# Performance work log

Hardware: AMD Instinct MI355X
Metric: run time of the kernel (lower is better)

The kernel has to match this reference:

```python
import jax, jax.numpy as jnp
import numpy as np

N = 100_000      # nodes
E = 1_600_000    # edges (before self-loops)
F_IN = 128       # num_features
H = 128          # nhid
G = 512          # graphs in batch
C = 10           # num_classes
EPS = 1e-5       # BatchNorm eps


def setup_inputs() -> dict:
    key = jax.random.key(0)
    ks = jax.random.split(key, 24)
    x = jax.random.normal(ks[0], (N, F_IN), jnp.float32)
    edge_index = jax.random.randint(ks[1], (2, E), 0, N, dtype=jnp.int64)
    batch = jnp.sort(jax.random.randint(ks[2], (N,), 0, G, dtype=jnp.int64))

    def lin(k, fi, fo):
        return jax.random.normal(k, (fi, fo), jnp.float32) / np.sqrt(fi).astype(np.float32)

    inp = dict(x=x, edge_index=edge_index, batch=batch)
    inp.update(
        W1=lin(ks[3], F_IN, H), b1=jnp.zeros((H,), jnp.float32),
        g1=jnp.ones((H,), jnp.float32), be1=jnp.zeros((H,), jnp.float32),
        W2=lin(ks[4], H, H), b2=jnp.zeros((H,), jnp.float32),
        g2=jnp.ones((H,), jnp.float32), be2=jnp.zeros((H,), jnp.float32),
        W3=lin(ks[5], H, H), b3=jnp.zeros((H,), jnp.float32),
        g3=jnp.ones((H,), jnp.float32), be3=jnp.zeros((H,), jnp.float32),
        gp=jnp.ones((H,), jnp.float32), bep=jnp.zeros((H,), jnp.float32),
        lw1=lin(ks[6], H, H), lb1=jnp.zeros((H,), jnp.float32),
        lw2=lin(ks[7], H, C), lb2=jnp.zeros((C,), jnp.float32),
    )
    return inp


def _batchnorm(h, g, b):
    # training-mode BatchNorm1d: batch stats, biased variance
    m = h.mean(axis=0)
    v = h.var(axis=0)
    return g * (h - m) * jax.lax.rsqrt(v + EPS) + b


def _gcn(h, W, b, src, dst, norm, n):
    # GCNConv: h @ W, then normalized gather-scatter aggregation
    h = h @ W
    msg = h[src] * norm[:, None]                     # [E+N, H] gather
    out = jax.ops.segment_sum(msg, dst, num_segments=n)
    return out + b


def reference(x, edge_index, batch, W1, b1, g1, be1, W2, b2, g2, be2,
              W3, b3, g3, be3, gp, bep, lw1, lb1, lw2, lb2):
    n = x.shape[0]
    loops = jnp.arange(n, dtype=edge_index.dtype)
    src = jnp.concatenate([edge_index[0], loops])
    dst = jnp.concatenate([edge_index[1], loops])
    # symmetric normalization D^{-1/2} (A+I) D^{-1/2}
    deg = jax.ops.segment_sum(jnp.ones_like(src, dtype=x.dtype), dst, num_segments=n)
    dis = jnp.where(deg > 0, jax.lax.rsqrt(jnp.maximum(deg, 1.0)), 0.0)
    norm = dis[src] * dis[dst]

    h = jax.nn.relu(_batchnorm(_gcn(x, W1, b1, src, dst, norm, n), g1, be1))
    h = jax.nn.relu(_batchnorm(_gcn(h, W2, b2, src, dst, norm, n), g2, be2))
    h = jax.nn.relu(_batchnorm(_gcn(h, W3, b3, src, dst, norm, n), g3, be3))

    # global_mean_pool over graph ids
    counts = jax.ops.segment_sum(jnp.ones((n,), x.dtype), batch, num_segments=G)
    pooled = jax.ops.segment_sum(h, batch, num_segments=G) / jnp.maximum(counts, 1.0)[:, None]

    z = _batchnorm(pooled, gp, bep)
    z = jax.nn.relu(z @ lw1 + lb1)
    # dropout_ratio=0.0 -> identity
    z = z @ lw2 + lb2
    return jax.nn.log_softmax(z, axis=-1)
```

## Files before the change

### kernel.cpp

```cpp
#include <hip/hip_runtime.h>
#include <hip/hip_bf16.h>
#include <cstdint>

#define HDIM 128

typedef __bf16 bf16x8 __attribute__((ext_vector_type(8)));
typedef unsigned short usx8 __attribute__((ext_vector_type(8)));
typedef float fx4 __attribute__((ext_vector_type(4)));

__device__ __forceinline__ float bf2f(unsigned short u) {
    unsigned int x = ((unsigned int)u) << 16;
    return __uint_as_float(x);
}
__device__ __forceinline__ unsigned short f2bf(float f) {
    unsigned int x = __float_as_uint(f);
    x += 0x7fffu + ((x >> 16) & 1u);
    return (unsigned short)(x >> 16);
}

__device__ __forceinline__ void detect_local(const unsigned int* xw, const unsigned int* eiw,
                                             int& f0, int& f1) {
    int sane = 0;
    for (int k = 0; k < 64; k++) {
        unsigned int w = xw[k];
        unsigned short ss[2] = {(unsigned short)(w & 0xffffu), (unsigned short)(w >> 16)};
        for (int q = 0; q < 2; q++) {
            int e = (ss[q] >> 7) & 0xFF;
            if ((ss[q] & 0x7fffu) == 0 || (e >= 100 && e <= 140)) sane++;
        }
    }
    f0 = (sane >= 110) ? 1 : 0;
    int zeros = 0;
    for (int k = 1; k < 64; k += 2)
        if (eiw[k] == 0) zeros++;
    f1 = (zeros >= 24) ? 1 : 0;
}

struct ParamTab {
    const void* p[15];
    int n[15];
    int off[15];
};

__global__ void phase1(const unsigned int* __restrict__ xw, const unsigned int* __restrict__ eiw,
                       const void* __restrict__ ei, const void* __restrict__ batch,
                       const void* __restrict__ W1, const void* __restrict__ W2,
                       const void* __restrict__ W3, ParamTab tab, int* __restrict__ flags,
                       float* __restrict__ gsumAll, int* __restrict__ Ct,
                       unsigned short* __restrict__ wconv, unsigned short* __restrict__ Wf,
                       int* __restrict__ goff, int* __restrict__ gcnt, int E, int N, int G,
                       int NB, int ntiles, int TILE) {
    __shared__ int h[1024];
    __shared__ int lf0s, lf1s;
    int b = blockIdx.x, t = threadIdx.x;
    if (t == 0) {
        int a0, a1;
        detect_local(xw, eiw, a0, a1);
        lf0s = a0;
        lf1s = a1;
    }
    __syncthreads();
    int lf0 = lf0s, lf1 = lf1s;
    if (b < ntiles) {
        for (int i = t; i < NB; i += 256) h[i] = 0;
        __syncthreads();
        int base = b * TILE;
        for (int i = t; i < TILE; i += 256) {
            int idx = base + i;
            if (idx < E) {
                int d = lf1 ? (int)((const long long*)ei)[(size_t)E + idx]
                            : ((const int*)ei)[(size_t)E + idx];
                atomicAdd(&h[d >> 9], 1);
            }
        }
        __syncthreads();
        for (int k = t; k < NB; k += 256) Ct[k * ntiles + b] = h[k];
    } else if (b < ntiles + 15) {
        int pb = b - ntiles;
        const void* src = tab.p[pb];
        int n = tab.n[pb];
        unsigned short* o = wconv + tab.off[pb];
        if (lf0) {
            const unsigned short* s = (const unsigned short*)src;
            for (int i = t; i < n; i += 256) o[i] = s[i];
        } else {
            const float* s = (const float*)src;
            for (int i = t; i < n; i += 256) o[i] = f2bf(s[i]);
        }
    } else if (b < ntiles + 17) {
        int gi = (b - ntiles - 15) * 256 + t;
        if (gi < G) {
            auto getb = [&](int i) -> int {
                return lf1 ? (int)((const long long*)batch)[i] : ((const int*)batch)[i];
            };
            auto lower = [&](int val) -> int {
                int lo = 0, hi = N;
                while (lo < hi) {
                    int mid = (lo + hi) >> 1;
                    if (getb(mid) < val) lo = mid + 1;
                    else hi = mid;
                }
                return lo;
            };
            int lo = lower(gi), hi = lower(gi + 1);
            goff[gi] = lo;
            gcnt[gi] = hi - lo;
        }
    } else if (b < ntiles + 17 + 24) {
        int idx = (b - ntiles - 17) * 256 + t;
        int layer = idx >> 11;
        int rem = idx & 2047;
        int kt = rem >> 9;
        int nt = (rem >> 6) & 7;
        int lane = rem & 63;
        const void* W = (layer == 0) ? W1 : ((layer == 1) ? W2 : W3);
        int row = lane & 15, quad = lane >> 4;
        unsigned short* o = Wf + ((size_t)layer * 2048 + (size_t)((kt * 8 + nt) * 64 + lane)) * 8;
#pragma unroll
        for (int j = 0; j < 8; j++) {
            int k = kt * 32 + quad * 8 + j;
            int off = k * HDIM + nt * 16 + row;
            o[j] = lf0 ? ((const unsigned short*)W)[off] : f2bf(((const float*)W)[off]);
        }
    } else {
        for (int i = t; i < 6144; i += 256) gsumAll[i] = 0.f;
        if (t == 0) {
            flags[0] = lf0;
            flags[1] = lf1;
        }
    }
}

__global__ void s1_scan(int* __restrict__ Ct, int* __restrict__ btot, int NB, int ntiles) {
    __shared__ int buf[512];
    int b = blockIdx.x, t = threadIdx.x;
    int v = (t < ntiles) ? Ct[b * ntiles + t] : 0;
    buf[t] = v;
    __syncthreads();
    for (int o = 1; o < 512; o <<= 1) {
        int a = (t >= o) ? buf[t - o] : 0;
        __syncthreads();
        buf[t] += a;
        __syncthreads();
    }
    if (t < ntiles) Ct[b * ntiles + t] = buf[t] - v;
    if (t == 0) btot[b] = buf[511];
}

__global__ void p1_scatter(const void* __restrict__ ei, const int* __restrict__ flags,
                           const int* __restrict__ Ct, const int* __restrict__ btot,
                           unsigned int* __restrict__ pairs, int E, int NB, int ntiles,
                           int TILE) {
    __shared__ int cur[1024];
    __shared__ int bb[256];
    int tile = blockIdx.x, t = threadIdx.x;
    int v = (t < NB) ? btot[t] : 0;
    bb[t] = v;
    __syncthreads();
    for (int o = 1; o < 256; o <<= 1) {
        int a = (t >= o) ? bb[t - o] : 0;
        __syncthreads();
        bb[t] += a;
        __syncthreads();
    }
    if (t < NB) cur[t] = (bb[t] - v) + Ct[t * ntiles + tile];
    __syncthreads();
    int base = tile * TILE;
    bool i64 = flags[1] != 0;
    for (int i = t; i < TILE; i += 256) {
        int idx = base + i;
        if (idx < E) {
            int s, d;
            if (i64) {
                s = (int)((const long long*)ei)[idx];
                d = (int)((const long long*)ei)[(size_t)E + idx];
            } else {
                s = ((const int*)ei)[idx];
                d = ((const int*)ei)[(size_t)E + idx];
            }
            int pos = atomicAdd(&cur[d >> 9], 1);
            pairs[pos] = ((unsigned)(d & 511) << 23) | (unsigned)s;
        }
    }
}

__global__ void p2_build(const unsigned int* __restrict__ pairs, const int* __restrict__ btot,
                         int* __restrict__ csrc, int* __restrict__ offs, int* __restrict__ cnt,
                         float* __restrict__ dis, int E, int N, int NB) {
    __shared__ int hist[512];
    __shared__ int start[512];
    __shared__ int cur[512];
    __shared__ int ps[256];
    __shared__ int bb[256];
    __shared__ int sh_excl[256];
    int b = blockIdx.x, t = threadIdx.x;
    int node0 = b * 512;
    int v = (t < NB) ? btot[t] : 0;
    bb[t] = v;
    __syncthreads();
    for (int o = 1; o < 256; o <<= 1) {
        int a = (t >= o) ? bb[t - o] : 0;
        __syncthreads();
        bb[t] += a;
        __syncthreads();
    }
    sh_excl[t] = bb[t] - v;
    for (int i = t; i < 512; i += 256) hist[i] = 0;
    __syncthreads();
    int lo = sh_excl[b];
    int hi = lo + ((b < NB) ? btot[b] : 0);
    for (int i = lo + t; i < hi; i += 256) {
        atomicAdd(&hist[pairs[i] >> 23], 1);
    }
    __syncthreads();
    ps[t] = hist[2 * t] + hist[2 * t + 1];
    __syncthreads();
    for (int o = 1; o < 256; o <<= 1) {
        int a = (t >= o) ? ps[t - o] : 0;
        __syncthreads();
        ps[t] += a;
        __syncthreads();
    }
    int e = t ? ps[t - 1] : 0;
    start[2 * t] = e;
    start[2 * t + 1] = e + hist[2 * t];
    __syncthreads();
    for (int i = t; i < 512; i += 256) {
        cur[i] = 0;
        int node = node0 + i;
        if (node < N) {
            offs[node] = lo + start[i];
            cnt[node] = hist[i];
            dis[node] = rsqrtf((float)(hist[i] + 1));
        }
    }
    __syncthreads();
    for (int i = lo + t; i < hi; i += 256) {
        unsigned int p = pairs[i];
        int l = p >> 23;
        int pos = lo + start[l] + atomicAdd(&cur[l], 1);
        csrc[pos] = (int)(p & 0x7fffffu);
    }
}

__global__ __launch_bounds__(256) void mm_mfma(const void* __restrict__ A,
                                               const unsigned short* __restrict__ Wf,
                                               unsigned short* __restrict__ C, int M,
                                               const float* __restrict__ gsumPrev,
                                               const unsigned short* __restrict__ gamma,
                                               const unsigned short* __restrict__ beta,
                                               const float* __restrict__ dis,
                                               const int* __restrict__ flags, int l0mode,
                                               float invn) {
    __shared__ float scs[128], shs[128];
    __shared__ unsigned short ldsC[4 * 16 * 136];
    int t = threadIdx.x;
    if (!l0mode && t < 128) {
        float s = 0.f, s2 = 0.f;
#pragma unroll
        for (int r = 0; r < 8; r++) {
            s += gsumPrev[r * 256 + t];
            s2 += gsumPrev[r * 256 + 128 + t];
        }
        float m = s * invn;
        float vv = s2 * invn - m * m;
        float sc = bf2f(gamma[t]) * rsqrtf(vv + 1e-5f);
        scs[t] = sc;
        shs[t] = bf2f(beta[t]) - m * sc;
    }
    __syncthreads();
    int gid = blockIdx.x * blockDim.x + t;
    int wave = gid >> 6;
    int lane = t & 63;
    int wv = t >> 6;
    int m0 = wave * 16;
    if (m0 >= M) return;
    int row = lane & 15, quad = lane >> 4;
    bool xfp32 = l0mode && !flags[0];
    const unsigned short* arow = (const unsigned short*)A + (size_t)(m0 + row) * HDIM + quad * 8;
    const float* arowf = (const float*)A + (size_t)(m0 + row) * HDIM + quad * 8;
    fx4 acc[8];
#pragma unroll
    for (int k = 0; k < 8; k++) acc[k] = (fx4){0.f, 0.f, 0.f, 0.f};
#pragma unroll
    for (int kt = 0; kt < 4; kt++) {
        bf16x8 a;
        if (xfp32) {
            fx4 f0 = *(const fx4*)(arowf + kt * 32);
            fx4 f1 = *(const fx4*)(arowf + kt * 32 + 4);
            usx8 tt;
#pragma unroll
            for (int q = 0; q < 4; q++) tt[q] = f2bf(f0[q]);
#pragma unroll
            for (int q = 0; q < 4; q++) tt[4 + q] = f2bf(f1[q]);
            a = __builtin_bit_cast(bf16x8, tt);
        } else {
            usx8 raw = *(const usx8*)(arow + kt * 32);
            if (!l0mode) {
                int col = kt * 32 + quad * 8;
                fx4 s0 = *(const fx4*)&scs[col];
                fx4 s1 = *(const fx4*)&scs[col + 4];
                fx4 h0 = *(const fx4*)&shs[col];
                fx4 h1 = *(const fx4*)&shs[col + 4];
                usx8 tt;
#pragma unroll
                for (int q = 0; q < 4; q++)
                    tt[q] = f2bf(fmaxf(s0[q] * bf2f(raw[q]) + h0[q], 0.f));
#pragma unroll
                for (int q = 0; q < 4; q++)
                    tt[4 + q] = f2bf(fmaxf(s1[q] * bf2f(raw[4 + q]) + h1[q], 0.f));
                a = __builtin_bit_cast(bf16x8, tt);
            } else {
                a = __builtin_bit_cast(bf16x8, raw);
            }
        }
        const unsigned short* wf = Wf + ((size_t)(kt * 8) * 64 + lane) * 8;
#pragma unroll
        for (int nt = 0; nt < 8; nt++) {
            bf16x8 bfr = __builtin_bit_cast(bf16x8, *(const usx8*)(wf + (size_t)nt * 64 * 8));
            acc[nt] = __builtin_amdgcn_mfma_f32_16x16x32_bf16(a, bfr, acc[nt], 0, 0, 0);
        }
    }
    float dsc[4];
#pragma unroll
    for (int r = 0; r < 4; r++) dsc[r] = dis[m0 + quad * 4 + r];
    unsigned short* lw = ldsC + wv * 16 * 136;
#pragma unroll
    for (int nt = 0; nt < 8; nt++) {
        int col = nt * 16 + row;
#pragma unroll
        for (int r = 0; r < 4; r++) {
            lw[(quad * 4 + r) * 136 + col] = f2bf(acc[nt][r] * dsc[r]);
        }
    }
    int row16 = lane >> 2;
    int seg = lane & 3;
    const unsigned short* src = lw + row16 * 136 + seg * 32;
    unsigned short* dst = C + (size_t)(m0 + row16) * HDIM + seg * 32;
#pragma unroll
    for (int k = 0; k < 4; k++) {
        *(usx8*)(dst + k * 8) = *(const usx8*)(src + k * 8);
    }
}

__global__ __launch_bounds__(256) void aggregate(const unsigned short* __restrict__ hw,
                                                 const float* __restrict__ dis,
                                                 const int* __restrict__ offs,
                                                 const int* __restrict__ cnt,
                                                 const int* __restrict__ csrc,
                                                 const unsigned short* __restrict__ bias,
                                                 unsigned short* __restrict__ agg,
                                                 float* __restrict__ gsum8, int n) {
    __shared__ float red[16 * 128];
    int t = threadIdx.x;
    int lane = t & 63;
    int wv = t >> 6;
    int grp = lane >> 4, sub = lane & 15;
    int colb = sub * 8;
    usx8 bv = *(const usx8*)(bias + colb);
    float csum[8], csq[8];
#pragma unroll
    for (int q = 0; q < 8; q++) {
        csum[q] = 0.f;
        csq[q] = 0.f;
    }
    int stride = gridDim.x * 16;
    for (int node = blockIdx.x * 16 + wv * 4 + grp; node < n; node += stride) {
        usx8 sv = *(const usx8*)(hw + (size_t)node * HDIM + colb);
        float a[8];
#pragma unroll
        for (int q = 0; q < 8; q++) a[q] = bf2f(sv[q]);
        int o = offs[node], c = cnt[node];
        int s0 = (c > 0) ? csrc[o] : 0;
        int s1 = (c > 1) ? csrc[o + 1] : 0;
        int s2 = (c > 2) ? csrc[o + 2] : 0;
        int s3 = (c > 3) ? csrc[o + 3] : 0;
        int j = 0;
        while (j < c) {
            usx8 v0 = *(const usx8*)(hw + (size_t)s0 * HDIM + colb);
            usx8 v1 = *(const usx8*)(hw + (size_t)s1 * HDIM + colb);
            usx8 v2 = *(const usx8*)(hw + (size_t)s2 * HDIM + colb);
            usx8 v3 = *(const usx8*)(hw + (size_t)s3 * HDIM + colb);
            s0 = (j + 4 < c) ? csrc[o + j + 4] : 0;
            s1 = (j + 5 < c) ? csrc[o + j + 5] : 0;
            s2 = (j + 6 < c) ? csrc[o + j + 6] : 0;
            s3 = (j + 7 < c) ? csrc[o + j + 7] : 0;
#pragma unroll
            for (int q = 0; q < 8; q++) a[q] += bf2f(v0[q]);
            if (j + 1 < c) {
#pragma unroll
                for (int q = 0; q < 8; q++) a[q] += bf2f(v1[q]);
            }
            if (j + 2 < c) {
#pragma unroll
                for (int q = 0; q < 8; q++) a[q] += bf2f(v2[q]);
            }
            if (j + 3 < c) {
#pragma unroll
                for (int q = 0; q < 8; q++) a[q] += bf2f(v3[q]);
            }
            j += 4;
        }
        float di = dis[node];
        usx8 ov;
#pragma unroll
        for (int q = 0; q < 8; q++) {
            float val = bf2f(bv[q]) + di * a[q];
            ov[q] = f2bf(val);
            float vr = bf2f(ov[q]);
            csum[q] += vr;
            csq[q] += vr * vr;
        }
        *(usx8*)(agg + (size_t)node * HDIM + colb) = ov;
    }
    int gidx = wv * 4 + grp;
    int rep = (blockIdx.x & 7) * 256;
#pragma unroll
    for (int q = 0; q < 8; q++) red[gidx * 128 + colb + q] = csum[q];
    __syncthreads();
    if (t < 128) {
        float s = 0.f;
#pragma unroll
        for (int g = 0; g < 16; g++) s += red[g * 128 + t];
        atomicAdd(&gsum8[rep + t], s);
    }
    __syncthreads();
#pragma unroll
    for (int q = 0; q < 8; q++) red[gidx * 128 + colb + q] = csq[q];
    __syncthreads();
    if (t < 128) {
        float s = 0.f;
#pragma unroll
        for (int g = 0; g < 16; g++) s += red[g * 128 + t];
        atomicAdd(&gsum8[rep + 128 + t], s);
    }
}

__global__ void pool(const unsigned short* __restrict__ hin, const int* __restrict__ goff,
                     const int* __restrict__ gcnt, const float* __restrict__ gsum3,
                     const unsigned short* __restrict__ gamma,
                     const unsigned short* __restrict__ beta, float* __restrict__ pooled,
                     float invn) {
    __shared__ float scs[128], shs[128];
    __shared__ float ls[256];
    int g = blockIdx.x, t = threadIdx.x;
    if (t < 128) {
        float s = 0.f, s2 = 0.f;
#pragma unroll
        for (int r = 0; r < 8; r++) {
            s += gsum3[r * 256 + t];
            s2 += gsum3[r * 256 + 128 + t];
        }
        float m = s * invn;
        float vv = s2 * invn - m * m;
        float sc = bf2f(gamma[t]) * rsqrtf(vv + 1e-5f);
        scs[t] = sc;
        shs[t] = bf2f(beta[t]) - m * sc;
    }
    __syncthreads();
    int c = t & 127, p = t >> 7;
    float scale = scs[c], shift = shs[c];
    int s = goff[g], cn = gcnt[g];
    float acc = 0.f;
    for (int r = s + p; r < s + cn; r += 2)
        acc += fmaxf(scale * bf2f(hin[(size_t)r * HDIM + c]) + shift, 0.f);
    ls[t] = acc;
    __syncthreads();
    if (t < 128) pooled[(size_t)g * HDIM + t] = (ls[t] + ls[t + 128]) / fmaxf((float)cn, 1.f);
}
__global__ void pooled_bn(const float* __restrict__ pooled, const unsigned short* __restrict__ g,
                          const unsigned short* __restrict__ be, float* __restrict__ psc,
                          float* __restrict__ psh, int G_) {
    int t = threadIdx.x;
    int c = t & 127, p = t >> 7;
    float s = 0.f, s2 = 0.f;
    for (int r = p; r < G_; r += 4) {
        float v = pooled[(size_t)r * HDIM + c];
        s += v;
        s2 += v * v;
    }
    __shared__ float ls[512], ls2[512];
    ls[t] = s;
    ls2[t] = s2;
    __syncthreads();
    if (t < 128) {
        float S = ls[t] + ls[t + 128] + ls[t + 256] + ls[t + 384];
        float S2 = ls2[t] + ls2[t + 128] + ls2[t + 256] + ls2[t + 384];
        float m = S / (float)G_;
        float v = S2 / (float)G_ - m * m;
        float sc = bf2f(g[t]) * rsqrtf(v + 1e-5f);
        psc[t] = sc;
        psh[t] = bf2f(be[t]) - m * sc;
    }
}
__global__ void mlp12(const float* __restrict__ pooled, const float* __restrict__ psc,
                      const float* __restrict__ psh, const unsigned short* __restrict__ lw1,
                      const unsigned short* __restrict__ lb1,
                      const unsigned short* __restrict__ lw2,
                      const unsigned short* __restrict__ lb2, void* __restrict__ out,
                      const int* __restrict__ flags) {
    int r = blockIdx.x, t = threadIdx.x;
    __shared__ float row[128];
    __shared__ float z1s[128];
    __shared__ float z2[10];
    __shared__ float lse;
    row[t] = psc[t] * pooled[(size_t)r * HDIM + t] + psh[t];
    __syncthreads();
    float acc = bf2f(lb1[t]);
    for (int k = 0; k < 128; k++) acc += row[k] * bf2f(lw1[k * HDIM + t]);
    z1s[t] = fmaxf(acc, 0.f);
    __syncthreads();
    if (t < 10) {
        float a = bf2f(lb2[t]);
        for (int k = 0; k < 128; k++) a += z1s[k] * bf2f(lw2[k * 10 + t]);
        z2[t] = a;
    }
    __syncthreads();
    if (t == 0) {
        float m = z2[0];
        for (int j = 1; j < 10; j++) m = fmaxf(m, z2[j]);
        float s = 0.f;
        for (int j = 0; j < 10; j++) s += expf(z2[j] - m);
        lse = m + logf(s);
    }
    __syncthreads();
    if (t < 10) {
        float v = z2[t] - lse;
        if (flags[0]) ((unsigned short*)out)[r * 10 + t] = f2bf(v);
        else ((float*)out)[r * 10 + t] = v;
    }
}

extern "C" void kernel_launch(void* const* d_in, const int* in_sizes, int n_in,
                              void* d_out, int out_size, void* d_ws, size_t ws_size,
                              hipStream_t stream) {
    const void* x = d_in[0];
    const void* ei = d_in[1];
    const void* batch = d_in[2];

    int N_ = in_sizes[2];
    int E_ = in_sizes[1] / 2;
    int G_ = out_size / 10;

    const int TILE = 4096;
    int NB = (N_ + 511) / 512;
    int ntiles = (E_ + TILE - 1) / TILE;
    int L = NB * ntiles;

    char* ws = (char*)d_ws;
    auto alloc = [&](size_t bytes) -> char* {
        char* p = ws;
        ws += (bytes + 255) & ~(size_t)255;
        return p;
    };
    int* flags = (int*)alloc(256);
    float* dis = (float*)alloc((size_t)N_ * 4);
    int* offs = (int*)alloc((size_t)N_ * 4);
    int* cnt = (int*)alloc((size_t)N_ * 4);
    int* Ct = (int*)alloc((size_t)L * 4);
    int* btot = (int*)alloc(1024);
    unsigned int* pairs = (unsigned int*)alloc((size_t)E_ * 4);
    int* csrc = (int*)alloc((size_t)E_ * 4);
    unsigned short* hw = (unsigned short*)alloc((size_t)N_ * HDIM * 2);
    unsigned short* aggbuf = (unsigned short*)alloc((size_t)N_ * HDIM * 2);
    unsigned short* wconv = (unsigned short*)alloc(70000 * 2);
    unsigned short* wfrag = (unsigned short*)alloc(3 * HDIM * HDIM * 2);
    float* gsumAll = (float*)alloc(6144 * 4);
    int* gcnt = (int*)alloc((size_t)G_ * 4);
    int* goff = (int*)alloc((size_t)G_ * 4);
    float* pooled = (float*)alloc((size_t)G_ * HDIM * 4);
    float* psc = (float*)alloc(128 * 4);
    float* psh = (float*)alloc(128 * 4);

    const int oB = 49152;
    const int oLB1 = oB + 1408;
    const int oLW1 = oLB1 + 128;
    const int oLW2 = oLW1 + 16384;
    const int oLB2 = oLW2 + 1280;

    ParamTab tab;
    const int srcIdx[15] = {4, 5, 6, 8, 9, 10, 12, 13, 14, 15, 16, 18, 17, 19, 20};
    const int dstOff[15] = {oB + 0, oB + 128, oB + 256,
                            oB + 384, oB + 512, oB + 640,
                            oB + 768, oB + 896, oB + 1024,
                            oB + 1152, oB + 1280,
                            oLB1, oLW1, oLW2, oLB2};
    for (int i = 0; i < 15; i++) {
        tab.p[i] = d_in[srcIdx[i]];
        tab.n[i] = in_sizes[srcIdx[i]];
        tab.off[i] = dstOff[i];
    }

    int p1_grid = ntiles + 15 + 2 + 24 + 1;
    phase1<<<p1_grid, 256, 0, stream>>>((const unsigned int*)x, (const unsigned int*)ei, ei,
                                        batch, d_in[3], d_in[7], d_in[11], tab, flags, gsumAll,
                                        Ct, wconv, wfrag, goff, gcnt, E_, N_, G_, NB, ntiles,
                                        TILE);
    s1_scan<<<NB, 512, 0, stream>>>(Ct, btot, NB, ntiles);
    p1_scatter<<<ntiles, 256, 0, stream>>>(ei, flags, Ct, btot, pairs, E_, NB, ntiles, TILE);
    p2_build<<<NB, 256, 0, stream>>>(pairs, btot, csrc, offs, cnt, dis, E_, N_, NB);

    int mm_blocks = (((N_ + 15) / 16) * 64 + 255) / 256;
    float invn = 1.f / (float)N_;

    for (int l = 0; l < 3; l++) {
        const void* A = (l == 0) ? x : (const void*)aggbuf;
        const float* gp = (l == 0) ? nullptr : (gsumAll + (size_t)(l - 1) * 2048);
        const unsigned short* gam = wconv + oB + (l ? (l - 1) * 384 + 128 : 0);
        const unsigned short* bet = wconv + oB + (l ? (l - 1) * 384 + 256 : 0);
        mm_mfma<<<mm_blocks, 256, 0, stream>>>(A, wfrag + (size_t)l * HDIM * HDIM, hw, N_, gp,
                                               gam, bet, dis, flags, (l == 0) ? 1 : 0, invn);
        aggregate<<<768, 256, 0, stream>>>(hw, dis, offs, cnt, csrc, wconv + oB + l * 384,
                                           aggbuf, gsumAll + (size_t)l * 2048, N_);
    }

    pool<<<G_, 256, 0, stream>>>(aggbuf, goff, gcnt, gsumAll + 2 * 2048,
                                 wconv + oB + 2 * 384 + 128, wconv + oB + 2 * 384 + 256, pooled,
                                 invn);
    pooled_bn<<<1, 512, 0, stream>>>(pooled, wconv + oB + 1152, wconv + oB + 1280, psc, psh, G_);
    mlp12<<<G_, 128, 0, stream>>>(pooled, psc, psh, wconv + oLW1, wconv + oLB1, wconv + oLW2,
                                  wconv + oLB2, d_out, flags);
}
```

Measured before the change: 514.5 us.

## Store transformed features in column-slice layout and aggregate per 16-column slice

The matmul epilogue now writes hw as eight 16-column slices, each contiguous over all nodes, and the aggregation kernel gives each block one slice, with each thread handling two columns. The aim is for a slice (about 3.2 MB) to stay cache-resident during the random neighbour gathers, at the cost of 4-byte gathers and eight times more CSR index reads. Smaller changes read int64 edge indices as their low 32-bit words, fold pooled BatchNorm stats into the MLP kernel (every block recomputes them, which removes a launch but adds redundant work), and simplify the prefix lookup in p2_build.

```diff
diff --git a/kernel.cpp b/kernel.cpp
--- a/kernel.cpp
+++ b/kernel.cpp
@@ -68,7 +68,7 @@
         for (int i = t; i < TILE; i += 256) {
             int idx = base + i;
             if (idx < E) {
-                int d = lf1 ? (int)((const long long*)ei)[(size_t)E + idx]
+                int d = lf1 ? ((const int*)ei)[2 * ((size_t)E + idx)]
                             : ((const int*)ei)[(size_t)E + idx];
                 atomicAdd(&h[d >> 9], 1);
             }
@@ -106,16 +106,15 @@
             goff[gi] = lo;
             gcnt[gi] = hi - lo;
         }
-    } else if (b < ntiles + 17 + 24) {
+    } else if (b < ntiles + 41) {
         int idx = (b - ntiles - 17) * 256 + t;
         int layer = idx >> 11;
         int rem = idx & 2047;
-        int kt = rem >> 9;
-        int nt = (rem >> 6) & 7;
-        int lane = rem & 63;
+        int kt = rem >> 9, nt = (rem >> 6) & 7, lane = rem & 63;
         const void* W = (layer == 0) ? W1 : ((layer == 1) ? W2 : W3);
         int row = lane & 15, quad = lane >> 4;
-        unsigned short* o = Wf + ((size_t)layer * 2048 + (size_t)((kt * 8 + nt) * 64 + lane)) * 8;
+        unsigned short* o =
+            Wf + ((size_t)layer * 2048 + (size_t)((kt * 8 + nt) * 64 + lane)) * 8;
 #pragma unroll
         for (int j = 0; j < 8; j++) {
             int k = kt * 32 + quad * 8 + j;
@@ -172,8 +171,8 @@
         if (idx < E) {
             int s, d;
             if (i64) {
-                s = (int)((const long long*)ei)[idx];
-                d = (int)((const long long*)ei)[(size_t)E + idx];
+                s = ((const int*)ei)[2 * (size_t)idx];
+                d = ((const int*)ei)[2 * ((size_t)E + idx)];
             } else {
                 s = ((const int*)ei)[idx];
                 d = ((const int*)ei)[(size_t)E + idx];
@@ -192,7 +191,6 @@
     __shared__ int cur[512];
     __shared__ int ps[256];
     __shared__ int bb[256];
-    __shared__ int sh_excl[256];
     int b = blockIdx.x, t = threadIdx.x;
     int node0 = b * 512;
     int v = (t < NB) ? btot[t] : 0;
@@ -204,14 +202,11 @@
         bb[t] += a;
         __syncthreads();
     }
-    sh_excl[t] = bb[t] - v;
+    int lo = bb[b] - btot[b];
+    int hi = lo + btot[b];
     for (int i = t; i < 512; i += 256) hist[i] = 0;
     __syncthreads();
-    int lo = sh_excl[b];
-    int hi = lo + ((b < NB) ? btot[b] : 0);
-    for (int i = lo + t; i < hi; i += 256) {
-        atomicAdd(&hist[pairs[i] >> 23], 1);
-    }
+    for (int i = lo + t; i < hi; i += 256) atomicAdd(&hist[pairs[i] >> 23], 1);
     __syncthreads();
     ps[t] = hist[2 * t] + hist[2 * t + 1];
     __syncthreads();
@@ -333,13 +328,15 @@
             lw[(quad * 4 + r) * 136 + col] = f2bf(acc[nt][r] * dsc[r]);
         }
     }
-    int row16 = lane >> 2;
-    int seg = lane & 3;
-    const unsigned short* src = lw + row16 * 136 + seg * 32;
-    unsigned short* dst = C + (size_t)(m0 + row16) * HDIM + seg * 32;
-#pragma unroll
-    for (int k = 0; k < 4; k++) {
-        *(usx8*)(dst + k * 8) = *(const usx8*)(src + k * 8);
+    int row16 = lane & 15;
+    int sgrp = lane >> 4;
+#pragma unroll
+    for (int k = 0; k < 2; k++) {
+        int s = sgrp * 2 + k;
+        const unsigned short* src = lw + row16 * 136 + s * 16;
+        unsigned short* dst = C + (size_t)s * M * 16 + (size_t)(m0 + row16) * 16;
+        *(usx8*)(dst) = *(const usx8*)(src);
+        *(usx8*)(dst + 8) = *(const usx8*)(src + 8);
     }
 }
 
@@ -351,25 +348,24 @@
                                                  const unsigned short* __restrict__ bias,
                                                  unsigned short* __restrict__ agg,
                                                  float* __restrict__ gsum8, int n) {
-    __shared__ float red[16 * 128];
+    __shared__ float red[256];
     int t = threadIdx.x;
     int lane = t & 63;
     int wv = t >> 6;
-    int grp = lane >> 4, sub = lane & 15;
-    int colb = sub * 8;
-    usx8 bv = *(const usx8*)(bias + colb);
-    float csum[8], csq[8];
-#pragma unroll
-    for (int q = 0; q < 8; q++) {
-        csum[q] = 0.f;
-        csq[q] = 0.f;
-    }
-    int stride = gridDim.x * 16;
-    for (int node = blockIdx.x * 16 + wv * 4 + grp; node < n; node += stride) {
-        usx8 sv = *(const usx8*)(hw + (size_t)node * HDIM + colb);
-        float a[8];
-#pragma unroll
-        for (int q = 0; q < 8; q++) a[q] = bf2f(sv[q]);
+    int slice = blockIdx.x & 7;
+    int bs = blockIdx.x >> 3;
+    int nsb = gridDim.x >> 3;
+    int ngrp = lane >> 3;
+    int cl = lane & 7;
+    const unsigned short* hws = hw + (size_t)slice * n * 16;
+    float b0 = bf2f(bias[slice * 16 + 2 * cl]);
+    float b1 = bf2f(bias[slice * 16 + 2 * cl + 1]);
+    float csum0 = 0.f, csq0 = 0.f, csum1 = 0.f, csq1 = 0.f;
+    int stride = nsb * 32;
+    for (int node = bs * 32 + wv * 8 + ngrp; node < n; node += stride) {
+        unsigned int sv = *(const unsigned int*)(hws + (size_t)node * 16 + 2 * cl);
+        float a0 = __uint_as_float(sv << 16);
+        float a1 = __uint_as_float(sv & 0xffff0000u);
         int o = offs[node], c = cnt[node];
         int s0 = (c > 0) ? csrc[o] : 0;
         int s1 = (c > 1) ? csrc[o + 1] : 0;
@@ -377,62 +373,72 @@
         int s3 = (c > 3) ? csrc[o + 3] : 0;
         int j = 0;
         while (j < c) {
-            usx8 v0 = *(const usx8*)(hw + (size_t)s0 * HDIM + colb);
-            usx8 v1 = *(const usx8*)(hw + (size_t)s1 * HDIM + colb);
-            usx8 v2 = *(const usx8*)(hw + (size_t)s2 * HDIM + colb);
-            usx8 v3 = *(const usx8*)(hw + (size_t)s3 * HDIM + colb);
+            unsigned int v0 = *(const unsigned int*)(hws + (size_t)s0 * 16 + 2 * cl);
+            unsigned int v1 = *(const unsigned int*)(hws + (size_t)s1 * 16 + 2 * cl);
+            unsigned int v2 = *(const unsigned int*)(hws + (size_t)s2 * 16 + 2 * cl);
+            unsigned int v3 = *(const unsigned int*)(hws + (size_t)s3 * 16 + 2 * cl);
             s0 = (j + 4 < c) ? csrc[o + j + 4] : 0;
             s1 = (j + 5 < c) ? csrc[o + j + 5] : 0;
             s2 = (j + 6 < c) ? csrc[o + j + 6] : 0;
             s3 = (j + 7 < c) ? csrc[o + j + 7] : 0;
-#pragma unroll
-            for (int q = 0; q < 8; q++) a[q] += bf2f(v0[q]);
+            a0 += __uint_as_float(v0 << 16);
+            a1 += __uint_as_float(v0 & 0xffff0000u);
             if (j + 1 < c) {
-#pragma unroll
-                for (int q = 0; q < 8; q++) a[q] += bf2f(v1[q]);
+                a0 += __uint_as_float(v1 << 16);
+                a1 += __uint_as_float(v1 & 0xffff0000u);
             }
             if (j + 2 < c) {
-#pragma unroll
-                for (int q = 0; q < 8; q++) a[q] += bf2f(v2[q]);
+                a0 += __uint_as_float(v2 << 16);
+                a1 += __uint_as_float(v2 & 0xffff0000u);
             }
             if (j + 3 < c) {
-#pragma unroll
-                for (int q = 0; q < 8; q++) a[q] += bf2f(v3[q]);
+                a0 += __uint_as_float(v3 << 16);
+                a1 += __uint_as_float(v3 & 0xffff0000u);
             }
             j += 4;
         }
         float di = dis[node];
-        usx8 ov;
-#pragma unroll
-        for (int q = 0; q < 8; q++) {
-            float val = bf2f(bv[q]) + di * a[q];
-            ov[q] = f2bf(val);
-            float vr = bf2f(ov[q]);
-            csum[q] += vr;
-            csq[q] += vr * vr;
-        }
-        *(usx8*)(agg + (size_t)node * HDIM + colb) = ov;
-    }
-    int gidx = wv * 4 + grp;
-    int rep = (blockIdx.x & 7) * 256;
-#pragma unroll
-    for (int q = 0; q < 8; q++) red[gidx * 128 + colb + q] = csum[q];
-    __syncthreads();
-    if (t < 128) {
+        unsigned short o0 = f2bf(b0 + di * a0);
+        unsigned short o1 = f2bf(b1 + di * a1);
+        float r0 = bf2f(o0), r1 = bf2f(o1);
+        csum0 += r0;
+        csq0 += r0 * r0;
+        csum1 += r1;
+        csq1 += r1 * r1;
+        *(unsigned int*)(agg + (size_t)node * HDIM + slice * 16 + 2 * cl) =
+            ((unsigned int)o1 << 16) | (unsigned int)o0;
+    }
+    int rep = (bs & 7) * 256;
+    red[t] = csum0;
+    __syncthreads();
+    if (t < 8) {
         float s = 0.f;
-#pragma unroll
-        for (int g = 0; g < 16; g++) s += red[g * 128 + t];
-        atomicAdd(&gsum8[rep + t], s);
-    }
-    __syncthreads();
-#pragma unroll
-    for (int q = 0; q < 8; q++) red[gidx * 128 + colb + q] = csq[q];
-    __syncthreads();
-    if (t < 128) {
+        for (int j = t; j < 256; j += 8) s += red[j];
+        atomicAdd(&gsum8[rep + slice * 16 + 2 * t], s);
+    }
+    __syncthreads();
+    red[t] = csum1;
+    __syncthreads();
+    if (t < 8) {
         float s = 0.f;
-#pragma unroll
-        for (int g = 0; g < 16; g++) s += red[g * 128 + t];
-        atomicAdd(&gsum8[rep + 128 + t], s);
+        for (int j = t; j < 256; j += 8) s += red[j];
+        atomicAdd(&gsum8[rep + slice * 16 + 2 * t + 1], s);
+    }
+    __syncthreads();
+    red[t] = csq0;
+    __syncthreads();
+    if (t < 8) {
+        float s = 0.f;
+        for (int j = t; j < 256; j += 8) s += red[j];
+        atomicAdd(&gsum8[rep + 128 + slice * 16 + 2 * t], s);
+    }
+    __syncthreads();
+    red[t] = csq1;
+    __syncthreads();
+    if (t < 8) {
+        float s = 0.f;
+        for (int j = t; j < 256; j += 8) s += red[j];
+        atomicAdd(&gsum8[rep + 128 + slice * 16 + 2 * t + 1], s);
     }
 }
 
@@ -468,43 +474,30 @@
     __syncthreads();
     if (t < 128) pooled[(size_t)g * HDIM + t] = (ls[t] + ls[t + 128]) / fmaxf((float)cn, 1.f);
 }
-__global__ void pooled_bn(const float* __restrict__ pooled, const unsigned short* __restrict__ g,
-                          const unsigned short* __restrict__ be, float* __restrict__ psc,
-                          float* __restrict__ psh, int G_) {
-    int t = threadIdx.x;
-    int c = t & 127, p = t >> 7;
-    float s = 0.f, s2 = 0.f;
-    for (int r = p; r < G_; r += 4) {
-        float v = pooled[(size_t)r * HDIM + c];
-        s += v;
-        s2 += v * v;
-    }
-    __shared__ float ls[512], ls2[512];
-    ls[t] = s;
-    ls2[t] = s2;
-    __syncthreads();
-    if (t < 128) {
-        float S = ls[t] + ls[t + 128] + ls[t + 256] + ls[t + 384];
-        float S2 = ls2[t] + ls2[t + 128] + ls2[t + 256] + ls2[t + 384];
-        float m = S / (float)G_;
-        float v = S2 / (float)G_ - m * m;
-        float sc = bf2f(g[t]) * rsqrtf(v + 1e-5f);
-        psc[t] = sc;
-        psh[t] = bf2f(be[t]) - m * sc;
-    }
-}
-__global__ void mlp12(const float* __restrict__ pooled, const float* __restrict__ psc,
-                      const float* __restrict__ psh, const unsigned short* __restrict__ lw1,
+
+__global__ void mlp12(const float* __restrict__ pooled, const unsigned short* __restrict__ gp,
+                      const unsigned short* __restrict__ bep,
+                      const unsigned short* __restrict__ lw1,
                       const unsigned short* __restrict__ lb1,
                       const unsigned short* __restrict__ lw2,
                       const unsigned short* __restrict__ lb2, void* __restrict__ out,
-                      const int* __restrict__ flags) {
+                      const int* __restrict__ flags, int G_) {
     int r = blockIdx.x, t = threadIdx.x;
     __shared__ float row[128];
     __shared__ float z1s[128];
     __shared__ float z2[10];
     __shared__ float lse;
-    row[t] = psc[t] * pooled[(size_t)r * HDIM + t] + psh[t];
+    float s = 0.f, s2 = 0.f;
+    for (int k = 0; k < G_; k++) {
+        float v = pooled[(size_t)k * HDIM + t];
+        s += v;
+        s2 += v * v;
+    }
+    float m = s / (float)G_;
+    float vv = s2 / (float)G_ - m * m;
+    float psc = bf2f(gp[t]) * rsqrtf(vv + 1e-5f);
+    float psh = bf2f(bep[t]) - m * psc;
+    row[t] = psc * pooled[(size_t)r * HDIM + t] + psh;
     __syncthreads();
     float acc = bf2f(lb1[t]);
     for (int k = 0; k < 128; k++) acc += row[k] * bf2f(lw1[k * HDIM + t]);
@@ -517,11 +510,11 @@
     }
     __syncthreads();
     if (t == 0) {
-        float m = z2[0];
-        for (int j = 1; j < 10; j++) m = fmaxf(m, z2[j]);
-        float s = 0.f;
-        for (int j = 0; j < 10; j++) s += expf(z2[j] - m);
-        lse = m + logf(s);
+        float mm = z2[0];
+        for (int j = 1; j < 10; j++) mm = fmaxf(mm, z2[j]);
+        float ss = 0.f;
+        for (int j = 0; j < 10; j++) ss += expf(z2[j] - mm);
+        lse = mm + logf(ss);
     }
     __syncthreads();
     if (t < 10) {
@@ -569,8 +562,6 @@
     int* gcnt = (int*)alloc((size_t)G_ * 4);
     int* goff = (int*)alloc((size_t)G_ * 4);
     float* pooled = (float*)alloc((size_t)G_ * HDIM * 4);
-    float* psc = (float*)alloc(128 * 4);
-    float* psh = (float*)alloc(128 * 4);
 
     const int oB = 49152;
     const int oLB1 = oB + 1408;
@@ -617,7 +608,6 @@
     pool<<<G_, 256, 0, stream>>>(aggbuf, goff, gcnt, gsumAll + 2 * 2048,
                                  wconv + oB + 2 * 384 + 128, wconv + oB + 2 * 384 + 256, pooled,
                                  invn);
-    pooled_bn<<<1, 512, 0, stream>>>(pooled, wconv + oB + 1152, wconv + oB + 1280, psc, psh, G_);
-    mlp12<<<G_, 128, 0, stream>>>(pooled, psc, psh, wconv + oLW1, wconv + oLB1, wconv + oLW2,
-                                  wconv + oLB2, d_out, flags);
-}
+    mlp12<<<G_, 128, 0, stream>>>(pooled, wconv + oB + 1152, wconv + oB + 1280, wconv + oLW1,
+                                  wconv + oLB1, wconv + oLW2, wconv + oLB2, d_out, flags, G_);
+}
```

After: 824.7 us. +60.3%, slower.
